# Optimization experiments

Hardware: AMD Instinct MI355X
Metric: run time of the kernel (lower is better)

The kernel has to match this reference:

```python
import jax, jax.numpy as jnp
import numpy as np

B, N, M, D = 32, 500, 500, 256
SQRT_D = 16.0
LOGIT_CLIP = 10.0


def setup_inputs() -> dict:
    key = jax.random.key(0)
    ks = jax.random.split(key, 12)
    s = 1.0 / np.sqrt(D)
    return {
        "encoded_q0": jax.random.normal(ks[0], (B, N, D), jnp.float32),
        "encoded_jobs": jax.random.normal(ks[1], (B, M, D), jnp.float32),
        "encoded_q1": jax.random.normal(ks[2], (B, N, D), jnp.float32),
        "cur_cost_mat": jax.random.uniform(ks[3], (B, N, M), jnp.float32),
        "log_scale": jnp.ones((1,), jnp.float32),
        "ninf_mask": jnp.zeros((B, N, M), jnp.float32),
        "Wq0": jax.random.normal(ks[4], (D, D), jnp.float32) * s,
        "Wq1": jax.random.normal(ks[5], (D, D), jnp.float32) * s,
        "Wk": jax.random.normal(ks[6], (D, D), jnp.float32) * s,
        "Wv": jax.random.normal(ks[7], (D, D), jnp.float32) * s,
        "alpha1": jnp.ones((1,), jnp.float32),
        "alpha2": jnp.ones((1,), jnp.float32),
    }


def reference(encoded_q0, encoded_jobs, encoded_q1, cur_cost_mat, log_scale,
              ninf_mask, Wq0, Wq1, Wk, Wv, alpha1, alpha2):
    # precomputed state (set_kv / set_q1): Linear without bias -> x @ W.T
    k = jnp.einsum('bmd,ed->bme', encoded_jobs, Wk)
    v = jnp.einsum('bmd,ed->bme', encoded_jobs, Wv)
    q1 = jnp.einsum('bnd,ed->bne', encoded_q1, Wq1)
    q0 = jnp.einsum('bnd,ed->bne', encoded_q0, Wq0)
    q = q1 + q0

    # AAFM: adaptation bias = -alpha1 * log_scale * cost (+ ninf_mask)
    exp_bias = jnp.exp(-alpha1 * log_scale * cur_cost_mat + ninf_mask)  # (B,N,M)
    exp_k = jnp.exp(k)                                                   # (B,M,D)
    num = jnp.einsum('bnm,bmd->bnd', exp_bias, exp_k * v)
    den = jnp.einsum('bnm,bmd->bnd', exp_bias, exp_k)
    weighted = jnp.nan_to_num(num / den)
    aafm_out = jax.nn.sigmoid(q) * weighted                              # (B,N,D)

    # single-head scoring against raw encoded_jobs
    score = jnp.einsum('bnd,bmd->bnm', aafm_out, encoded_jobs)
    score = score / SQRT_D - alpha2 * log_scale * cur_cost_mat
    score = LOGIT_CLIP * jnp.tanh(score) + ninf_mask
    return jax.nn.softmax(score, axis=-1)
```

## Files before the change

### kernel.cpp

```cpp
#include <hip/hip_runtime.h>
#include <math.h>

using u16 = unsigned short;
typedef __attribute__((ext_vector_type(8))) short short8;
typedef __attribute__((ext_vector_type(16))) float floatx16;

constexpr int Bc = 32, Nn = 500, Mm = 500, Dd = 256;
constexpr float LOGIT_CLIP = 10.0f;
constexpr float INV_SQRT_D = 1.0f / 16.0f;

__device__ __forceinline__ floatx16 mfma32(short8 a, short8 b, floatx16 c) {
    return __builtin_amdgcn_mfma_f32_32x32x16_bf16(a, b, c, 0, 0, 0);
}

__device__ __forceinline__ floatx16 zero16() {
    floatx16 v = {0.f,0.f,0.f,0.f,0.f,0.f,0.f,0.f,0.f,0.f,0.f,0.f,0.f,0.f,0.f,0.f};
    return v;
}

__device__ __forceinline__ void split1(float x, u16& h, u16& l) {
    unsigned u = __float_as_uint(x);
    unsigned rh = (u + 0x7FFFu + ((u >> 16) & 1u)) & 0xFFFF0000u;
    float fh = __uint_as_float(rh);
    float fl = x - fh;
    unsigned ul = __float_as_uint(fl);
    unsigned rl = ul + 0x7FFFu + ((ul >> 16) & 1u);
    h = (u16)(rh >> 16);
    l = (u16)(rl >> 16);
}

__device__ __forceinline__ u16 bf16rtn(float x) {
    unsigned u = __float_as_uint(x);
    return (u16)((u + 0x7FFFu + ((u >> 16) & 1u)) >> 16);
}

__device__ __forceinline__ float fast_tanh(float x) {
    return 1.0f - 2.0f / (__expf(2.0f * x) + 1.0f);
}

__device__ __forceinline__ void split8(const float4& a, const float4& c,
                                       short8& hv, short8& lv) {
    u16 hh, ll;
    split1(a.x, hh, ll); hv[0] = (short)hh; lv[0] = (short)ll;
    split1(a.y, hh, ll); hv[1] = (short)hh; lv[1] = (short)ll;
    split1(a.z, hh, ll); hv[2] = (short)hh; lv[2] = (short)ll;
    split1(a.w, hh, ll); hv[3] = (short)hh; lv[3] = (short)ll;
    split1(c.x, hh, ll); hv[4] = (short)hh; lv[4] = (short)ll;
    split1(c.y, hh, ll); hv[5] = (short)hh; lv[5] = (short)ll;
    split1(c.z, hh, ll); hv[6] = (short)hh; lv[6] = (short)ll;
    split1(c.w, hh, ll); hv[7] = (short)hh; lv[7] = (short)ll;
}


__global__ __launch_bounds__(256) void k0w_pk(const float* __restrict__ s0,
                                              const float* __restrict__ s1,
                                              const float* __restrict__ s2,
                                              const float* __restrict__ s3,
                                              u16* __restrict__ pkw) {
    const float* s = blockIdx.y == 0 ? s0 : blockIdx.y == 1 ? s1 :
                     blockIdx.y == 2 ? s2 : s3;
    const int w = blockIdx.y;
    const int flat = (blockIdx.x * 256 + threadIdx.x) * 8;
    const int i = flat >> 8, j0 = flat & 255;
    float4 a = *(const float4*)&s[flat];
    float4 c = *(const float4*)&s[flat + 4];
    short8 hv, lv;
    split8(a, c, hv, lv);
    const int dt = i >> 5, i31 = i & 31, dc = j0 >> 4, hp = (j0 >> 3) & 1;
    const size_t off = (size_t)(w * 8 + dt) * 16384 + (size_t)dc * 1024
                     + (size_t)((hp << 5) | i31) * 8;
    *(short8*)&pkw[off] = hv;
    *(short8*)&pkw[off + 512] = lv;
}

__global__ __launch_bounds__(512) void k1_kv(const float* __restrict__ jobs,
                                             const u16* __restrict__ pkw,
                                             u16* __restrict__ pkj,
                                             u16* __restrict__ pkb) {
    __shared__ u16 tq[2][32][264];
    const int t = threadIdx.x;
    const int lane = t & 63, wv = t >> 6;
    const int l31 = lane & 31, h = lane >> 5;
    const int mt = blockIdx.x;
    const int b = blockIdx.y;
    const int M0 = mt * 32;

#pragma unroll
    for (int it = 0; it < 2; ++it) {
        const int flat = (it * 512 + t) * 8;
        const int nl = flat >> 8, j0 = flat & 255;
        const int m = M0 + nl;
        short8 hv = {0,0,0,0,0,0,0,0}, lv = {0,0,0,0,0,0,0,0};
        if (m < Mm) {
            const size_t o = ((size_t)b * Mm + m) * Dd + j0;
            float4 a = *(const float4*)&jobs[o];
            float4 c = *(const float4*)&jobs[o + 4];
            split8(a, c, hv, lv);
        }
        *(short8*)&tq[0][nl][j0] = hv;
        *(short8*)&tq[1][nl][j0] = lv;
    }
    __syncthreads();

    {
        u16* dst = pkj + (size_t)(b * 16 + mt) * 16384;
#pragma unroll
        for (int it = 0; it < 4; ++it) {
            const int u = it * 512 + t;
            const int dc = u >> 7;
            const int rem = u & 127;
            const int sel = rem >> 6;
            const int idx = rem & 63;
            const int hp = idx >> 5, r31 = idx & 31;
            short8 v = *(const short8*)&tq[sel][r31][dc * 16 + hp * 8];
            *(short8*)&dst[(size_t)dc * 1024 + sel * 512 + (size_t)idx * 8] = v;
        }
    }

    const int dt = wv;
    const size_t wk  = (size_t)dt * 16384 + (size_t)lane * 8;
    const size_t wvb = (size_t)(8 + dt) * 16384 + (size_t)lane * 8;

    floatx16 ak = zero16(), av = zero16();

    short8 buf[3][4];
#define K1L(S, DC) { \
    buf[S][0] = *(const short8*)(pkw + wk  + (size_t)(DC) * 1024); \
    buf[S][1] = *(const short8*)(pkw + wk  + (size_t)(DC) * 1024 + 512); \
    buf[S][2] = *(const short8*)(pkw + wvb + (size_t)(DC) * 1024); \
    buf[S][3] = *(const short8*)(pkw + wvb + (size_t)(DC) * 1024 + 512); }

    K1L(0, 0)
    K1L(1, 1)
#pragma unroll
    for (int it = 0; it < 16; ++it) {
        if (it + 2 < 16) { K1L((it + 2) % 3, it + 2) }
        const int c = it % 3;
        const int co = it * 16 + h * 8;
        short8 jH = *(const short8*)&tq[0][l31][co];
        short8 jL = *(const short8*)&tq[1][l31][co];
        ak = mfma32(buf[c][0], jH, ak);
        ak = mfma32(buf[c][0], jL, ak);
        ak = mfma32(buf[c][1], jH, ak);
        av = mfma32(buf[c][2], jH, av);
        av = mfma32(buf[c][2], jL, av);
        av = mfma32(buf[c][3], jH, av);
    }
#undef K1L

    const int hp = (l31 >> 3) & 1, ee = l31 & 7, mcl = l31 >> 4;
    const size_t sb0 = ((size_t)b * 8 + dt) * 65536
                     + (size_t)(mt * 2 + mcl) * 2048 + (size_t)hp * 256 + ee;
    const bool v0 = (M0 + l31) < Mm;
#pragma unroll
    for (int r = 0; r < 16; ++r) {
        const int d31 = (r & 3) + ((r >> 2) << 3) + (h << 2);
        const size_t o = sb0 + (size_t)d31 * 8;
        u16 hh, ll;
        const float ek = v0 ? __expf(ak[r]) : 0.f;
        const float ev = v0 ? ek * av[r] : 0.f;
        split1(ek, hh, ll); pkb[o] = hh; pkb[o + 512] = ll;
        split1(ev, hh, ll); pkb[o + 1024] = hh; pkb[o + 1536] = ll;
    }
}

__global__ __launch_bounds__(512) void k2_q(const float* __restrict__ q0,
                                            const float* __restrict__ q1,
                                            const u16* __restrict__ pkw,
                                            float* __restrict__ sq) {
    __shared__ u16 tq[4][32][264];
    const int t = threadIdx.x;
    const int lane = t & 63, wv = t >> 6;
    const int l31 = lane & 31, h = lane >> 5;
    const int b = blockIdx.y;
    const int nt = blockIdx.x;

#pragma unroll
    for (int s = 0; s < 2; ++s) {
        const float* src = s ? q1 : q0;
#pragma unroll
        for (int it = 0; it < 2; ++it) {
            const int flat = (it * 512 + t) * 8;
            const int nl = flat >> 8, j0 = flat & 255;
            const int n = min(nt * 32 + nl, Nn - 1);
            const size_t o = ((size_t)b * Nn + n) * Dd + j0;
            float4 a = *(const float4*)&src[o];
            float4 c = *(const float4*)&src[o + 4];
            short8 hv, lv;
            split8(a, c, hv, lv);
            *(short8*)&tq[s * 2][nl][j0] = hv;
            *(short8*)&tq[s * 2 + 1][nl][j0] = lv;
        }
    }
    __syncthreads();

    const int dt = wv;
    const size_t w0b = (size_t)(16 + dt) * 16384 + (size_t)lane * 8;
    const size_t w1b = (size_t)(24 + dt) * 16384 + (size_t)lane * 8;

    floatx16 acc = zero16();

    short8 buf[3][4];
#define K2L(S, DC) { \
    buf[S][0] = *(const short8*)(pkw + w0b + (size_t)(DC) * 1024); \
    buf[S][1] = *(const short8*)(pkw + w0b + (size_t)(DC) * 1024 + 512); \
    buf[S][2] = *(const short8*)(pkw + w1b + (size_t)(DC) * 1024); \
    buf[S][3] = *(const short8*)(pkw + w1b + (size_t)(DC) * 1024 + 512); }

    K2L(0, 0)
    K2L(1, 1)
#pragma unroll
    for (int it = 0; it < 16; ++it) {
        if (it + 2 < 16) { K2L((it + 2) % 3, it + 2) }
        const int c = it % 3;
        const int co = it * 16 + h * 8;
        short8 a0h = *(const short8*)&tq[0][l31][co];
        short8 a0l = *(const short8*)&tq[1][l31][co];
        short8 a1h = *(const short8*)&tq[2][l31][co];
        short8 a1l = *(const short8*)&tq[3][l31][co];
        acc = mfma32(a0h, buf[c][0], acc);
        acc = mfma32(a0h, buf[c][1], acc);
        acc = mfma32(a0l, buf[c][0], acc);
        acc = mfma32(a1h, buf[c][2], acc);
        acc = mfma32(a1h, buf[c][3], acc);
        acc = mfma32(a1l, buf[c][2], acc);
    }
#undef K2L

    float* sp = sq + ((((size_t)b * 16 + nt) * 8 + dt) * 64 + lane) * 16;
#pragma unroll
    for (int r = 0; r < 16; ++r) {
        sp[r] = 1.0f / (1.0f + __expf(-acc[r]));
    }
}

__global__ __launch_bounds__(512) void k34(const float* __restrict__ cost,
                                           const float* __restrict__ mask,
                                           const float* __restrict__ alpha1,
                                           const float* __restrict__ alpha2,
                                           const float* __restrict__ lsc,
                                           const u16* __restrict__ pkb,
                                           const u16* __restrict__ pkj,
                                           const float* __restrict__ sq,
                                           float* __restrict__ out) {
    __shared__ u16 sh[16640];
    __shared__ float pred[32][8];
    const int i = blockIdx.x;
    const int x = i & 7, j = i >> 3;
    const int nt = j & 15;
    const int b = ((j >> 4) << 3) + x;
    const int t = threadIdx.x;
    const int lane = t & 63, wv = t >> 6;
    const int l31 = lane & 31, h = lane >> 5;
    const int N0 = nt << 5;

    const float a1ls = alpha1[0] * lsc[0];
#pragma unroll
    for (int q = 0; q < 4; ++q) {
        const int flat = (q << 12) + (t << 3);
        const int nl = flat >> 9, m = flat & 511;
        const int n = min(N0 + nl, Nn - 1);
        const size_t o = ((size_t)b * Nn + n) * Mm + m;
        ushort4 w0 = {0, 0, 0, 0}, w1 = {0, 0, 0, 0};
        if (m <= 488) {
            float4 c0 = *(const float4*)&cost[o];
            float4 c1 = *(const float4*)&cost[o + 4];
            float4 k0 = *(const float4*)&mask[o];
            float4 k1 = *(const float4*)&mask[o + 4];
            w0.x = bf16rtn(__expf(fmaf(-a1ls, c0.x, k0.x)));
            w0.y = bf16rtn(__expf(fmaf(-a1ls, c0.y, k0.y)));
            w0.z = bf16rtn(__expf(fmaf(-a1ls, c0.z, k0.z)));
            w0.w = bf16rtn(__expf(fmaf(-a1ls, c0.w, k0.w)));
            w1.x = bf16rtn(__expf(fmaf(-a1ls, c1.x, k1.x)));
            w1.y = bf16rtn(__expf(fmaf(-a1ls, c1.y, k1.y)));
            w1.z = bf16rtn(__expf(fmaf(-a1ls, c1.z, k1.z)));
            w1.w = bf16rtn(__expf(fmaf(-a1ls, c1.w, k1.w)));
        } else if (m == 496) {
            float4 c0 = *(const float4*)&cost[o];
            float4 k0 = *(const float4*)&mask[o];
            w0.x = bf16rtn(__expf(fmaf(-a1ls, c0.x, k0.x)));
            w0.y = bf16rtn(__expf(fmaf(-a1ls, c0.y, k0.y)));
            w0.z = bf16rtn(__expf(fmaf(-a1ls, c0.z, k0.z)));
            w0.w = bf16rtn(__expf(fmaf(-a1ls, c0.w, k0.w)));
        }
        *(ushort4*)&sh[nl * 520 + m] = w0;
        *(ushort4*)&sh[nl * 520 + m + 4] = w1;
    }
    __syncthreads();

    const size_t bbase = ((size_t)b * 8 + wv) * 65536 + (size_t)lane * 8;
    floatx16 dn = zero16(), nm = zero16();
    short8 buf[3][4];
#define K3L(S, MC) { \
    buf[S][0] = *(const short8*)(pkb + bbase + (size_t)(MC) * 2048); \
    buf[S][1] = *(const short8*)(pkb + bbase + (size_t)(MC) * 2048 + 512); \
    buf[S][2] = *(const short8*)(pkb + bbase + (size_t)(MC) * 2048 + 1024); \
    buf[S][3] = *(const short8*)(pkb + bbase + (size_t)(MC) * 2048 + 1536); }

    K3L(0, 0)
    K3L(1, 1)
#pragma unroll
    for (int mc = 0; mc < 32; ++mc) {
        if (mc + 2 < 32) { K3L((mc + 2) % 3, mc + 2) }
        const int c = mc % 3;
        short8 aa = *(const short8*)&sh[l31 * 520 + mc * 16 + h * 8];
        dn = mfma32(aa, buf[c][0], dn);
        dn = mfma32(aa, buf[c][1], dn);
        nm = mfma32(aa, buf[c][2], nm);
        nm = mfma32(aa, buf[c][3], nm);
    }
#undef K3L
    __syncthreads();

    {
        const float* sp = sq + ((((size_t)b * 16 + nt) * 8 + wv) * 64 + lane) * 16;
        const int hp = (l31 >> 3) & 1, ee = l31 & 7;
        const int fo = (wv * 2 + (l31 >> 4)) * 1024 + hp * 256 + ee;
#pragma unroll
        for (int r = 0; r < 16; ++r) {
            const int n31 = (r & 3) + ((r >> 2) << 3) + (h << 2);
            const float d0 = dn[r];
            const float w0 = (d0 != 0.f) ? nm[r] / d0 : 0.f;
            u16 hh, ll;
            split1(sp[r] * w0, hh, ll);
            sh[fo + n31 * 8] = hh;
            sh[fo + 512 + n31 * 8] = ll;
        }
    }
    __syncthreads();

    const u16* jb0p = pkj + ((size_t)b * 16 + wv * 2) * 16384 + (size_t)lane * 8;
    const u16* jb1p = jb0p + 16384;
    const int m0g = wv * 64 + l31;
    const int m1g = m0g + 32;

    floatx16 acc0 = zero16(), acc1 = zero16();
    short8 jbuf[3][4];
#define K4L(S, DC) { \
    jbuf[S][0] = *(const short8*)(jb0p + (size_t)(DC) * 1024); \
    jbuf[S][1] = *(const short8*)(jb0p + (size_t)(DC) * 1024 + 512); \
    jbuf[S][2] = *(const short8*)(jb1p + (size_t)(DC) * 1024); \
    jbuf[S][3] = *(const short8*)(jb1p + (size_t)(DC) * 1024 + 512); }

    K4L(0, 0)
    K4L(1, 1)
#pragma unroll
    for (int dc = 0; dc < 16; ++dc) {
        if (dc + 2 < 16) { K4L((dc + 2) % 3, dc + 2) }
        const int c = dc % 3;
        short8 aH = *(const short8*)&sh[dc * 1024 + lane * 8];
        short8 aL = *(const short8*)&sh[dc * 1024 + 512 + lane * 8];
        acc0 = mfma32(aH, jbuf[c][0], acc0);
        acc0 = mfma32(aH, jbuf[c][1], acc0);
        acc0 = mfma32(aL, jbuf[c][0], acc0);
        acc1 = mfma32(aH, jbuf[c][2], acc1);
        acc1 = mfma32(aH, jbuf[c][3], acc1);
        acc1 = mfma32(aL, jbuf[c][2], acc1);
    }
#undef K4L

    float lg0[16], lg1[16];
    const float a2ls = alpha2[0] * lsc[0];
    const size_t cb = (size_t)b * Nn * Mm;
#pragma unroll
    for (int r = 0; r < 16; ++r) {
        const int row = (r & 3) + ((r >> 2) << 3) + (h << 2);
        const int n = N0 + row;
        if (n < Nn) {
            const size_t o = cb + (size_t)n * Mm + m0g;
            lg0[r] = LOGIT_CLIP * fast_tanh(fmaf(-a2ls, cost[o], acc0[r] * INV_SQRT_D)) + mask[o];
            if (m1g < Mm) {
                const size_t o1 = o + 32;
                lg1[r] = LOGIT_CLIP * fast_tanh(fmaf(-a2ls, cost[o1], acc1[r] * INV_SQRT_D)) + mask[o1];
            } else lg1[r] = -1e30f;
        } else { lg0[r] = -1e30f; lg1[r] = -1e30f; }
    }

    float rm[16];
#pragma unroll
    for (int r = 0; r < 16; ++r) rm[r] = fmaxf(lg0[r], lg1[r]);
#pragma unroll
    for (int d = 1; d < 32; d <<= 1)
#pragma unroll
        for (int r = 0; r < 16; ++r) rm[r] = fmaxf(rm[r], __shfl_xor(rm[r], d));
    if (l31 == 0) {
#pragma unroll
        for (int r = 0; r < 16; ++r)
            pred[(r & 3) + ((r >> 2) << 3) + (h << 2)][wv] = rm[r];
    }
    __syncthreads();
    float fm[16];
#pragma unroll
    for (int r = 0; r < 16; ++r) {
        const int row = (r & 3) + ((r >> 2) << 3) + (h << 2);
        float v = pred[row][0];
#pragma unroll
        for (int w = 1; w < 8; ++w) v = fmaxf(v, pred[row][w]);
        fm[r] = v;
    }
    __syncthreads();

    float sm[16];
#pragma unroll
    for (int r = 0; r < 16; ++r) {
        lg0[r] = __expf(lg0[r] - fm[r]);
        lg1[r] = __expf(lg1[r] - fm[r]);
        sm[r] = lg0[r] + lg1[r];
    }
#pragma unroll
    for (int d = 1; d < 32; d <<= 1)
#pragma unroll
        for (int r = 0; r < 16; ++r) sm[r] += __shfl_xor(sm[r], d);
    if (l31 == 0) {
#pragma unroll
        for (int r = 0; r < 16; ++r)
            pred[(r & 3) + ((r >> 2) << 3) + (h << 2)][wv] = sm[r];
    }
    __syncthreads();

#pragma unroll
    for (int r = 0; r < 16; ++r) {
        const int row = (r & 3) + ((r >> 2) << 3) + (h << 2);
        const int n = N0 + row;
        if (n < Nn) {
            float s = pred[row][0];
#pragma unroll
            for (int w = 1; w < 8; ++w) s += pred[row][w];
            const float inv = 1.0f / s;
            const size_t o = cb + (size_t)n * Mm + m0g;
            out[o] = lg0[r] * inv;
            if (m1g < Mm) out[o + 32] = lg1[r] * inv;
        }
    }
}

extern "C" void kernel_launch(void* const* d_in, const int* in_sizes, int n_in,
                              void* d_out, int out_size, void* d_ws, size_t ws_size,
                              hipStream_t stream) {
    const float* q0        = (const float*)d_in[0];
    const float* jobs      = (const float*)d_in[1];
    const float* q1        = (const float*)d_in[2];
    const float* cost      = (const float*)d_in[3];
    const float* log_scale = (const float*)d_in[4];
    const float* mask      = (const float*)d_in[5];
    const float* Wq0       = (const float*)d_in[6];
    const float* Wq1       = (const float*)d_in[7];
    const float* Wk        = (const float*)d_in[8];
    const float* Wv        = (const float*)d_in[9];
    const float* alpha1    = (const float*)d_in[10];
    const float* alpha2    = (const float*)d_in[11];
    float* out = (float*)d_out;

    const size_t PK_SZ  = (size_t)Bc * 16 * 16384;
    const size_t PKW_SZ = (size_t)4 * 8 * 16384;
    const size_t PKB_SZ = (size_t)Bc * 8 * 65536;

    u16* ws   = (u16*)d_ws;
    u16* pkj  = ws;
    u16* pkw  = ws + PK_SZ;
    u16* pkb  = pkw + PKW_SZ;
    float* sq = (float*)(pkb + PKB_SZ);
    (void)ws_size;

    k0w_pk<<<dim3(32, 4), dim3(256), 0, stream>>>(Wk, Wv, Wq0, Wq1, pkw);
    k1_kv<<<dim3(16, 32), dim3(512), 0, stream>>>(jobs, pkw, pkj, pkb);
    k2_q<<<dim3(16, 32), dim3(512), 0, stream>>>(q0, q1, pkw, sq);
    k34<<<512, dim3(512), 0, stream>>>(cost, mask, alpha1, alpha2, log_scale,
                                       pkb, pkj, sq, out);
}
```

Before: 263.9 us.

## Merge KV and Q projection kernels into one launch; prefetch cost/mask early

The separate k1_kv and k2_q kernels are merged into a single k12 launch that uses blockIdx.z to choose the KV or Q path. The Q path now stages q0 and q1 one at a time through a half-sized shared buffer, which cuts LDS use at the cost of an extra barrier. In k34, cost and mask values are loaded into registers before the final MFMA loop so their global latency overlaps the matmul, and the jobs prefetch buffer is reduced from triple to double buffering. The aim is less launch overhead and better latency hiding, in exchange for higher register pressure in k34.

```diff
diff --git a/kernel.cpp b/kernel.cpp
--- a/kernel.cpp
+++ b/kernel.cpp
@@ -73,164 +73,151 @@
     *(short8*)&pkw[off + 512] = lv;
 }
 
-__global__ __launch_bounds__(512) void k1_kv(const float* __restrict__ jobs,
-                                             const u16* __restrict__ pkw,
-                                             u16* __restrict__ pkj,
-                                             u16* __restrict__ pkb) {
+__global__ __launch_bounds__(512) void k12(const float* __restrict__ jobs,
+                                           const float* __restrict__ q0,
+                                           const float* __restrict__ q1,
+                                           const u16* __restrict__ pkw,
+                                           u16* __restrict__ pkj,
+                                           u16* __restrict__ pkb,
+                                           float* __restrict__ sq) {
     __shared__ u16 tq[2][32][264];
     const int t = threadIdx.x;
     const int lane = t & 63, wv = t >> 6;
     const int l31 = lane & 31, h = lane >> 5;
-    const int mt = blockIdx.x;
+    const int tile = blockIdx.x;
     const int b = blockIdx.y;
-    const int M0 = mt * 32;
-
-#pragma unroll
-    for (int it = 0; it < 2; ++it) {
-        const int flat = (it * 512 + t) * 8;
-        const int nl = flat >> 8, j0 = flat & 255;
-        const int m = M0 + nl;
-        short8 hv = {0,0,0,0,0,0,0,0}, lv = {0,0,0,0,0,0,0,0};
-        if (m < Mm) {
-            const size_t o = ((size_t)b * Mm + m) * Dd + j0;
-            float4 a = *(const float4*)&jobs[o];
-            float4 c = *(const float4*)&jobs[o + 4];
-            split8(a, c, hv, lv);
-        }
-        *(short8*)&tq[0][nl][j0] = hv;
-        *(short8*)&tq[1][nl][j0] = lv;
-    }
-    __syncthreads();
-
-    {
-        u16* dst = pkj + (size_t)(b * 16 + mt) * 16384;
-#pragma unroll
-        for (int it = 0; it < 4; ++it) {
-            const int u = it * 512 + t;
-            const int dc = u >> 7;
-            const int rem = u & 127;
-            const int sel = rem >> 6;
-            const int idx = rem & 63;
-            const int hp = idx >> 5, r31 = idx & 31;
-            short8 v = *(const short8*)&tq[sel][r31][dc * 16 + hp * 8];
-            *(short8*)&dst[(size_t)dc * 1024 + sel * 512 + (size_t)idx * 8] = v;
-        }
-    }
-
-    const int dt = wv;
-    const size_t wk  = (size_t)dt * 16384 + (size_t)lane * 8;
-    const size_t wvb = (size_t)(8 + dt) * 16384 + (size_t)lane * 8;
-
-    floatx16 ak = zero16(), av = zero16();
-
-    short8 buf[3][4];
-#define K1L(S, DC) { \
-    buf[S][0] = *(const short8*)(pkw + wk  + (size_t)(DC) * 1024); \
-    buf[S][1] = *(const short8*)(pkw + wk  + (size_t)(DC) * 1024 + 512); \
-    buf[S][2] = *(const short8*)(pkw + wvb + (size_t)(DC) * 1024); \
-    buf[S][3] = *(const short8*)(pkw + wvb + (size_t)(DC) * 1024 + 512); }
-
-    K1L(0, 0)
-    K1L(1, 1)
-#pragma unroll
-    for (int it = 0; it < 16; ++it) {
-        if (it + 2 < 16) { K1L((it + 2) % 3, it + 2) }
-        const int c = it % 3;
-        const int co = it * 16 + h * 8;
-        short8 jH = *(const short8*)&tq[0][l31][co];
-        short8 jL = *(const short8*)&tq[1][l31][co];
-        ak = mfma32(buf[c][0], jH, ak);
-        ak = mfma32(buf[c][0], jL, ak);
-        ak = mfma32(buf[c][1], jH, ak);
-        av = mfma32(buf[c][2], jH, av);
-        av = mfma32(buf[c][2], jL, av);
-        av = mfma32(buf[c][3], jH, av);
-    }
-#undef K1L
-
-    const int hp = (l31 >> 3) & 1, ee = l31 & 7, mcl = l31 >> 4;
-    const size_t sb0 = ((size_t)b * 8 + dt) * 65536
-                     + (size_t)(mt * 2 + mcl) * 2048 + (size_t)hp * 256 + ee;
-    const bool v0 = (M0 + l31) < Mm;
-#pragma unroll
-    for (int r = 0; r < 16; ++r) {
-        const int d31 = (r & 3) + ((r >> 2) << 3) + (h << 2);
-        const size_t o = sb0 + (size_t)d31 * 8;
-        u16 hh, ll;
-        const float ek = v0 ? __expf(ak[r]) : 0.f;
-        const float ev = v0 ? ek * av[r] : 0.f;
-        split1(ek, hh, ll); pkb[o] = hh; pkb[o + 512] = ll;
-        split1(ev, hh, ll); pkb[o + 1024] = hh; pkb[o + 1536] = ll;
-    }
-}
-
-__global__ __launch_bounds__(512) void k2_q(const float* __restrict__ q0,
-                                            const float* __restrict__ q1,
-                                            const u16* __restrict__ pkw,
-                                            float* __restrict__ sq) {
-    __shared__ u16 tq[4][32][264];
-    const int t = threadIdx.x;
-    const int lane = t & 63, wv = t >> 6;
-    const int l31 = lane & 31, h = lane >> 5;
-    const int b = blockIdx.y;
-    const int nt = blockIdx.x;
-
-#pragma unroll
-    for (int s = 0; s < 2; ++s) {
-        const float* src = s ? q1 : q0;
+
+    if (blockIdx.z == 0) {
+        const int mt = tile;
+        const int M0 = mt * 32;
+
 #pragma unroll
         for (int it = 0; it < 2; ++it) {
             const int flat = (it * 512 + t) * 8;
             const int nl = flat >> 8, j0 = flat & 255;
-            const int n = min(nt * 32 + nl, Nn - 1);
-            const size_t o = ((size_t)b * Nn + n) * Dd + j0;
-            float4 a = *(const float4*)&src[o];
-            float4 c = *(const float4*)&src[o + 4];
-            short8 hv, lv;
-            split8(a, c, hv, lv);
-            *(short8*)&tq[s * 2][nl][j0] = hv;
-            *(short8*)&tq[s * 2 + 1][nl][j0] = lv;
-        }
-    }
-    __syncthreads();
-
-    const int dt = wv;
-    const size_t w0b = (size_t)(16 + dt) * 16384 + (size_t)lane * 8;
-    const size_t w1b = (size_t)(24 + dt) * 16384 + (size_t)lane * 8;
-
-    floatx16 acc = zero16();
-
-    short8 buf[3][4];
+            const int m = M0 + nl;
+            short8 hv = {0,0,0,0,0,0,0,0}, lv = {0,0,0,0,0,0,0,0};
+            if (m < Mm) {
+                const size_t o = ((size_t)b * Mm + m) * Dd + j0;
+                float4 a = *(const float4*)&jobs[o];
+                float4 c = *(const float4*)&jobs[o + 4];
+                split8(a, c, hv, lv);
+            }
+            *(short8*)&tq[0][nl][j0] = hv;
+            *(short8*)&tq[1][nl][j0] = lv;
+        }
+        __syncthreads();
+
+        {
+            u16* dst = pkj + (size_t)(b * 16 + mt) * 16384;
+#pragma unroll
+            for (int it = 0; it < 4; ++it) {
+                const int u = it * 512 + t;
+                const int dc = u >> 7;
+                const int rem = u & 127;
+                const int sel = rem >> 6;
+                const int idx = rem & 63;
+                const int hp = idx >> 5, r31 = idx & 31;
+                short8 v = *(const short8*)&tq[sel][r31][dc * 16 + hp * 8];
+                *(short8*)&dst[(size_t)dc * 1024 + sel * 512 + (size_t)idx * 8] = v;
+            }
+        }
+
+        const int dt = wv;
+        const size_t wk  = (size_t)dt * 16384 + (size_t)lane * 8;
+        const size_t wvb = (size_t)(8 + dt) * 16384 + (size_t)lane * 8;
+
+        floatx16 ak = zero16(), av = zero16();
+
+        short8 buf[3][4];
+#define K1L(S, DC) { \
+        buf[S][0] = *(const short8*)(pkw + wk  + (size_t)(DC) * 1024); \
+        buf[S][1] = *(const short8*)(pkw + wk  + (size_t)(DC) * 1024 + 512); \
+        buf[S][2] = *(const short8*)(pkw + wvb + (size_t)(DC) * 1024); \
+        buf[S][3] = *(const short8*)(pkw + wvb + (size_t)(DC) * 1024 + 512); }
+
+        K1L(0, 0)
+        K1L(1, 1)
+#pragma unroll
+        for (int it = 0; it < 16; ++it) {
+            if (it + 2 < 16) { K1L((it + 2) % 3, it + 2) }
+            const int c = it % 3;
+            const int co = it * 16 + h * 8;
+            short8 jH = *(const short8*)&tq[0][l31][co];
+            short8 jL = *(const short8*)&tq[1][l31][co];
+            ak = mfma32(buf[c][0], jH, ak);
+            ak = mfma32(buf[c][0], jL, ak);
+            ak = mfma32(buf[c][1], jH, ak);
+            av = mfma32(buf[c][2], jH, av);
+            av = mfma32(buf[c][2], jL, av);
+            av = mfma32(buf[c][3], jH, av);
+        }
+#undef K1L
+
+        const int hp = (l31 >> 3) & 1, ee = l31 & 7, mcl = l31 >> 4;
+        const size_t sb0 = ((size_t)b * 8 + dt) * 65536
+                         + (size_t)(mt * 2 + mcl) * 2048 + (size_t)hp * 256 + ee;
+        const bool v0 = (M0 + l31) < Mm;
+#pragma unroll
+        for (int r = 0; r < 16; ++r) {
+            const int d31 = (r & 3) + ((r >> 2) << 3) + (h << 2);
+            const size_t o = sb0 + (size_t)d31 * 8;
+            u16 hh, ll;
+            const float ek = v0 ? __expf(ak[r]) : 0.f;
+            const float ev = v0 ? ek * av[r] : 0.f;
+            split1(ek, hh, ll); pkb[o] = hh; pkb[o + 512] = ll;
+            split1(ev, hh, ll); pkb[o + 1024] = hh; pkb[o + 1536] = ll;
+        }
+    } else {
+        const int nt = tile;
+        const int dt = wv;
+        floatx16 acc = zero16();
+
+#pragma unroll
+        for (int s = 0; s < 2; ++s) {
+            const float* src = s ? q1 : q0;
+            if (s) __syncthreads();
+#pragma unroll
+            for (int it = 0; it < 2; ++it) {
+                const int flat = (it * 512 + t) * 8;
+                const int nl = flat >> 8, j0 = flat & 255;
+                const int n = min(nt * 32 + nl, Nn - 1);
+                const size_t o = ((size_t)b * Nn + n) * Dd + j0;
+                float4 a = *(const float4*)&src[o];
+                float4 c = *(const float4*)&src[o + 4];
+                short8 hv, lv;
+                split8(a, c, hv, lv);
+                *(short8*)&tq[0][nl][j0] = hv;
+                *(short8*)&tq[1][nl][j0] = lv;
+            }
+            __syncthreads();
+
+            const size_t wb = (size_t)(16 + s * 8 + dt) * 16384 + (size_t)lane * 8;
+            short8 buf[3][2];
 #define K2L(S, DC) { \
-    buf[S][0] = *(const short8*)(pkw + w0b + (size_t)(DC) * 1024); \
-    buf[S][1] = *(const short8*)(pkw + w0b + (size_t)(DC) * 1024 + 512); \
-    buf[S][2] = *(const short8*)(pkw + w1b + (size_t)(DC) * 1024); \
-    buf[S][3] = *(const short8*)(pkw + w1b + (size_t)(DC) * 1024 + 512); }
-
-    K2L(0, 0)
-    K2L(1, 1)
-#pragma unroll
-    for (int it = 0; it < 16; ++it) {
-        if (it + 2 < 16) { K2L((it + 2) % 3, it + 2) }
-        const int c = it % 3;
-        const int co = it * 16 + h * 8;
-        short8 a0h = *(const short8*)&tq[0][l31][co];
-        short8 a0l = *(const short8*)&tq[1][l31][co];
-        short8 a1h = *(const short8*)&tq[2][l31][co];
-        short8 a1l = *(const short8*)&tq[3][l31][co];
-        acc = mfma32(a0h, buf[c][0], acc);
-        acc = mfma32(a0h, buf[c][1], acc);
-        acc = mfma32(a0l, buf[c][0], acc);
-        acc = mfma32(a1h, buf[c][2], acc);
-        acc = mfma32(a1h, buf[c][3], acc);
-        acc = mfma32(a1l, buf[c][2], acc);
-    }
+            buf[S][0] = *(const short8*)(pkw + wb + (size_t)(DC) * 1024); \
+            buf[S][1] = *(const short8*)(pkw + wb + (size_t)(DC) * 1024 + 512); }
+            K2L(0, 0)
+            K2L(1, 1)
+#pragma unroll
+            for (int it = 0; it < 16; ++it) {
+                if (it + 2 < 16) { K2L((it + 2) % 3, it + 2) }
+                const int c = it % 3;
+                const int co = it * 16 + h * 8;
+                short8 aH = *(const short8*)&tq[0][l31][co];
+                short8 aL = *(const short8*)&tq[1][l31][co];
+                acc = mfma32(aH, buf[c][0], acc);
+                acc = mfma32(aH, buf[c][1], acc);
+                acc = mfma32(aL, buf[c][0], acc);
+            }
 #undef K2L
-
-    float* sp = sq + ((((size_t)b * 16 + nt) * 8 + dt) * 64 + lane) * 16;
-#pragma unroll
-    for (int r = 0; r < 16; ++r) {
-        sp[r] = 1.0f / (1.0f + __expf(-acc[r]));
+        }
+
+        float* sp = sq + ((((size_t)b * 16 + nt) * 8 + dt) * 64 + lane) * 16;
+#pragma unroll
+        for (int r = 0; r < 16; ++r) {
+            sp[r] = 1.0f / (1.0f + __expf(-acc[r]));
+        }
     }
 }
 
@@ -329,13 +316,25 @@
     }
     __syncthreads();
 
+    const int m0g = wv * 64 + l31;
+    const int m1g = m0g + 32;
+    const size_t cb = (size_t)b * Nn * Mm;
+    float cst0[16], msk0[16], cst1[16], msk1[16];
+#pragma unroll
+    for (int r = 0; r < 16; ++r) {
+        const int row = (r & 3) + ((r >> 2) << 3) + (h << 2);
+        const int nc = min(N0 + row, Nn - 1);
+        const size_t o = cb + (size_t)nc * Mm + m0g;
+        cst0[r] = cost[o]; msk0[r] = mask[o];
+        if (m1g < Mm) { cst1[r] = cost[o + 32]; msk1[r] = mask[o + 32]; }
+        else { cst1[r] = 0.f; msk1[r] = 0.f; }
+    }
+
     const u16* jb0p = pkj + ((size_t)b * 16 + wv * 2) * 16384 + (size_t)lane * 8;
     const u16* jb1p = jb0p + 16384;
-    const int m0g = wv * 64 + l31;
-    const int m1g = m0g + 32;
 
     floatx16 acc0 = zero16(), acc1 = zero16();
-    short8 jbuf[3][4];
+    short8 jbuf[2][4];
 #define K4L(S, DC) { \
     jbuf[S][0] = *(const short8*)(jb0p + (size_t)(DC) * 1024); \
     jbuf[S][1] = *(const short8*)(jb0p + (size_t)(DC) * 1024 + 512); \
@@ -343,35 +342,31 @@
     jbuf[S][3] = *(const short8*)(jb1p + (size_t)(DC) * 1024 + 512); }
 
     K4L(0, 0)
-    K4L(1, 1)
 #pragma unroll
     for (int dc = 0; dc < 16; ++dc) {
-        if (dc + 2 < 16) { K4L((dc + 2) % 3, dc + 2) }
-        const int c = dc % 3;
+        const int cur = dc & 1;
+        if (dc + 1 < 16) { K4L(cur ^ 1, dc + 1) }
         short8 aH = *(const short8*)&sh[dc * 1024 + lane * 8];
         short8 aL = *(const short8*)&sh[dc * 1024 + 512 + lane * 8];
-        acc0 = mfma32(aH, jbuf[c][0], acc0);
-        acc0 = mfma32(aH, jbuf[c][1], acc0);
-        acc0 = mfma32(aL, jbuf[c][0], acc0);
-        acc1 = mfma32(aH, jbuf[c][2], acc1);
-        acc1 = mfma32(aH, jbuf[c][3], acc1);
-        acc1 = mfma32(aL, jbuf[c][2], acc1);
+        acc0 = mfma32(aH, jbuf[cur][0], acc0);
+        acc0 = mfma32(aH, jbuf[cur][1], acc0);
+        acc0 = mfma32(aL, jbuf[cur][0], acc0);
+        acc1 = mfma32(aH, jbuf[cur][2], acc1);
+        acc1 = mfma32(aH, jbuf[cur][3], acc1);
+        acc1 = mfma32(aL, jbuf[cur][2], acc1);
     }
 #undef K4L
 
     float lg0[16], lg1[16];
     const float a2ls = alpha2[0] * lsc[0];
-    const size_t cb = (size_t)b * Nn * Mm;
 #pragma unroll
     for (int r = 0; r < 16; ++r) {
         const int row = (r & 3) + ((r >> 2) << 3) + (h << 2);
         const int n = N0 + row;
         if (n < Nn) {
-            const size_t o = cb + (size_t)n * Mm + m0g;
-            lg0[r] = LOGIT_CLIP * fast_tanh(fmaf(-a2ls, cost[o], acc0[r] * INV_SQRT_D)) + mask[o];
+            lg0[r] = LOGIT_CLIP * fast_tanh(fmaf(-a2ls, cst0[r], acc0[r] * INV_SQRT_D)) + msk0[r];
             if (m1g < Mm) {
-                const size_t o1 = o + 32;
-                lg1[r] = LOGIT_CLIP * fast_tanh(fmaf(-a2ls, cost[o1], acc1[r] * INV_SQRT_D)) + mask[o1];
+                lg1[r] = LOGIT_CLIP * fast_tanh(fmaf(-a2ls, cst1[r], acc1[r] * INV_SQRT_D)) + msk1[r];
             } else lg1[r] = -1e30f;
         } else { lg0[r] = -1e30f; lg1[r] = -1e30f; }
     }
@@ -463,8 +458,7 @@
     (void)ws_size;
 
     k0w_pk<<<dim3(32, 4), dim3(256), 0, stream>>>(Wk, Wv, Wq0, Wq1, pkw);
-    k1_kv<<<dim3(16, 32), dim3(512), 0, stream>>>(jobs, pkw, pkj, pkb);
-    k2_q<<<dim3(16, 32), dim3(512), 0, stream>>>(q0, q1, pkw, sq);
+    k12<<<dim3(16, 32, 2), dim3(512), 0, stream>>>(jobs, q0, q1, pkw, pkj, pkb, sq);
     k34<<<512, dim3(512), 0, stream>>>(cost, mask, alpha1, alpha2, log_scale,
                                        pkb, pkj, sq, out);
 }
```

After: 271.8 us. 1.03x slower.
